# Kernel optimization log

Measured on AMD Instinct MI355X. Metric: run time of the kernel, lower is better.

Reference implementation:

```python
import jax, jax.numpy as jnp
import numpy as np

NUM_USERS = 100000
NUM_ITEMS = 50000
EMB = 64
B = 8192
MAXM = 50
ATT_H = 16
PRED_H = 8


def setup_inputs() -> dict:
    key = jax.random.key(0)
    ks = jax.random.split(key, 12)
    member_idx = jax.random.randint(ks[0], (B, MAXM), 0, NUM_USERS)
    # ragged group sizes in [1, MAXM]
    lens = jax.random.randint(ks[1], (B,), 1, MAXM + 1)
    member_mask = jnp.arange(MAXM)[None, :] < lens[:, None]  # bool [B, M]
    item_inputs = jax.random.randint(ks[2], (B,), 0, NUM_ITEMS)
    s = 1.0 / np.sqrt(EMB)
    user_table = jax.random.normal(ks[3], (NUM_USERS, EMB), jnp.float32) * s
    item_table = jax.random.normal(ks[4], (NUM_ITEMS, EMB), jnp.float32) * s
    att_w1 = jax.random.normal(ks[5], (2 * EMB, ATT_H), jnp.float32) * 0.05
    att_b1 = jnp.zeros((ATT_H,), jnp.float32)
    att_w2 = jax.random.normal(ks[6], (ATT_H, 1), jnp.float32) * 0.05
    att_b2 = jnp.zeros((1,), jnp.float32)
    pred_w1 = jax.random.normal(ks[7], (3 * EMB, PRED_H), jnp.float32) * 0.05
    pred_b1 = jnp.zeros((PRED_H,), jnp.float32)
    pred_w2 = jax.random.normal(ks[8], (PRED_H, 1), jnp.float32) * 0.05
    pred_b2 = jnp.zeros((1,), jnp.float32)
    return dict(member_idx=member_idx, member_mask=member_mask, item_inputs=item_inputs,
                user_table=user_table, item_table=item_table,
                att_w1=att_w1, att_b1=att_b1, att_w2=att_w2, att_b2=att_b2,
                pred_w1=pred_w1, pred_b1=pred_b1, pred_w2=pred_w2, pred_b2=pred_b2)


def reference(member_idx, member_mask, item_inputs, user_table, item_table,
              att_w1, att_b1, att_w2, att_b2, pred_w1, pred_b1, pred_w2, pred_b2):
    mem_e = user_table[member_idx]            # [B, M, d]
    item_e = item_table[item_inputs]          # [B, d]
    # attention MLP over concat(member, item)
    cat = jnp.concatenate(
        [mem_e, jnp.broadcast_to(item_e[:, None, :], mem_e.shape)], axis=-1)  # [B, M, 2d]
    h = jax.nn.relu(jnp.einsum('bmf,fh->bmh', cat, att_w1) + att_b1)
    logits = (jnp.einsum('bmh,ho->bmo', h, att_w2) + att_b2)[..., 0]          # [B, M]
    logits = jnp.where(member_mask, logits, -jnp.inf)
    wts = jax.nn.softmax(logits, axis=-1)                                     # [B, M]
    g = jnp.einsum('bm,bmd->bd', wts, mem_e)                                  # [B, d]
    new = jnp.concatenate([g * item_e, g, item_e], axis=-1)                   # [B, 3d]
    ph = jax.nn.relu(new @ pred_w1 + pred_b1)
    y = jax.nn.sigmoid(ph @ pred_w2 + pred_b2)                                # [B, 1]
    return y
```

## Files before the change

kernel.cpp:

```cpp
#include <hip/hip_runtime.h>
#include <hip/hip_bf16.h>


__global__ void AGREE_12773232738622_probe(
    const void* member_mask,
    const void* user_table,
    int* ws)
{
    if (ws[2] == 0x5AFE0001) return;

    const int lane = threadIdx.x;
    const int wi = lane >> 4;
    const int r  = lane & 15;

    int len = 0, ok = 1, prev = 1;
    for (int m = 0; m < 50; ++m) {
        long e = 50L * r + m;
        int nz;
        if (wi == 0)      nz = (((const unsigned char*)member_mask)[e] != 0);
        else if (wi == 1) nz = (((const unsigned short*)member_mask)[e] != 0);
        else if (wi == 2) nz = (((const unsigned int*)member_mask)[e] != 0u);
        else {
            const unsigned int* p = (const unsigned int*)member_mask;
            nz = ((p[2 * e] | p[2 * e + 1]) != 0u);
        }
        if (nz && !prev) ok = 0;
        if (nz) len = len + 1;
        prev = nz;
    }
    if (len == 0) ok = 0;

    ok = ok & __shfl_xor(ok, 1);
    ok = ok & __shfl_xor(ok, 2);
    ok = ok & __shfl_xor(ok, 4);
    ok = ok & __shfl_xor(ok, 8);
    int mx = len;
    mx = max(mx, __shfl_xor(mx, 1));
    mx = max(mx, __shfl_xor(mx, 2));
    mx = max(mx, __shfl_xor(mx, 4));
    mx = max(mx, __shfl_xor(mx, 8));

    int o0 = __shfl(ok, 0),  o1 = __shfl(ok, 16), o2 = __shfl(ok, 32), o3 = __shfl(ok, 48);
    int L0 = __shfl(mx, 0),  L1 = __shfl(mx, 16), L2 = __shfl(mx, 32), L3 = __shfl(mx, 48);

    float v = __bfloat162float(((const __hip_bfloat16*)user_table)[lane]);
    float a = (v < 0.0f) ? -v : v;
    int huge = (!(a < 4.0f)) ? 1 : 0;
    unsigned long long hb = __ballot(huge);
    int hcnt = __popcll(hb);

    if (lane == 0) {
        int bestW = 1, bestLen = -1;
        if (o0 && L0 > bestLen) { bestLen = L0; bestW = 1; }
        if (o1 && L1 > bestLen) { bestLen = L1; bestW = 2; }
        if (o2 && L2 > bestLen) { bestLen = L2; bestW = 4; }
        if (o3 && L3 > bestLen) { bestLen = L3; bestW = 8; }
        ws[0] = bestW;
        ws[1] = (hcnt >= 8) ? 1 : 0;
        ws[2] = 0x5AFE0001;
    }
}

__global__ __launch_bounds__(256, 4) void AGREE_12773232738622_kernel(
    const int* member_idx,
    const void* member_mask,
    const int* item_inputs,
    const void* user_table,
    const void* item_table,
    const void* att_w1,
    const void* att_b1,
    const void* att_w2,
    const void* att_b2,
    const void* pred_w1,
    const void* pred_b1,
    const void* pred_w2,
    const void* pred_b2,
    void* out,
    const int* ws)
{
    const int tid  = threadIdx.x;
    const int lane = tid & 63;
    const int wave = tid >> 6;
    const int b    = blockIdx.x * 4 + wave;
    const int mode = ws[0];
    const int isf  = ws[1];

    int valid = 0;
    if (lane < 50) {
        long e0 = 50L * b + lane;
        if (mode == 1)      valid = (((const unsigned char*)member_mask)[e0] != 0);
        else if (mode == 2) valid = (((const unsigned short*)member_mask)[e0] != 0);
        else if (mode == 4) valid = (((const unsigned int*)member_mask)[e0] != 0u);
        else {
            const unsigned int* p = (const unsigned int*)member_mask;
            valid = ((p[2 * e0] | p[2 * e0 + 1]) != 0u);
        }
    }
    unsigned long long vm = __ballot(valid);
    int len = __popcll(vm);
    if (len < 1)  len = 1;
    if (len > 50) len = 50;

    const int item_id = item_inputs[b];
    float itemv;
    if (isf) itemv = ((const float*)item_table)[item_id * 64 + lane];
    else     itemv = __bfloat162float(((const __hip_bfloat16*)item_table)[item_id * 64 + lane]);

    int idxv = 0;
    if (lane < 50) idxv = member_idx[b * 50 + lane];

    float part;
    {
        const int kk = lane & 15;
        const int c  = lane >> 4;
        if (isf) part = (c == 0) ? ((const float*)att_b1)[kk] : 0.0f;
        else     part = (c == 0) ? __bfloat162float(((const __hip_bfloat16*)att_b1)[kk]) : 0.0f;
        for (int t = 0; t < 16; ++t) {
            int f = c * 16 + t;
            float iv = __shfl(itemv, f);
            float w;
            if (isf) w = ((const float*)att_w1)[(64 + f) * 16 + kk];
            else     w = __bfloat162float(((const __hip_bfloat16*)att_w1)[(64 + f) * 16 + kk]);
            part += iv * w;
        }
        part += __shfl_xor(part, 16);
        part += __shfl_xor(part, 32);
    }
    float h[16];
    #pragma unroll
    for (int k = 0; k < 16; ++k) h[k] = __shfl(part, k);

    if (lane < len) {
        if (isf) {
            const float* rp = (const float*)user_table + (long)idxv * 64;
            const float* w1 = (const float*)att_w1;
            float4 vv[16];
            #pragma unroll
            for (int c = 0; c < 16; ++c) vv[c] = ((const float4*)rp)[c];
            #pragma unroll
            for (int c = 0; c < 16; ++c) {
                #pragma unroll
                for (int k = 0; k < 16; ++k) {
                    h[k] += vv[c].x * w1[(c * 4 + 0) * 16 + k];
                    h[k] += vv[c].y * w1[(c * 4 + 1) * 16 + k];
                    h[k] += vv[c].z * w1[(c * 4 + 2) * 16 + k];
                    h[k] += vv[c].w * w1[(c * 4 + 3) * 16 + k];
                }
            }
        } else {
            const unsigned short* rp = (const unsigned short*)user_table + (long)idxv * 64;
            const unsigned int* w1u = (const unsigned int*)att_w1;
            uint4 vv[8];
            #pragma unroll
            for (int c = 0; c < 8; ++c) vv[c] = ((const uint4*)rp)[c];
            #pragma unroll
            for (int c = 0; c < 8; ++c) {
                float e[8];
                e[0] = __uint_as_float(vv[c].x << 16);
                e[1] = __uint_as_float(vv[c].x & 0xFFFF0000u);
                e[2] = __uint_as_float(vv[c].y << 16);
                e[3] = __uint_as_float(vv[c].y & 0xFFFF0000u);
                e[4] = __uint_as_float(vv[c].z << 16);
                e[5] = __uint_as_float(vv[c].z & 0xFFFF0000u);
                e[6] = __uint_as_float(vv[c].w << 16);
                e[7] = __uint_as_float(vv[c].w & 0xFFFF0000u);
                #pragma unroll
                for (int j = 0; j < 8; ++j) {
                    #pragma unroll
                    for (int p = 0; p < 8; ++p) {
                        unsigned int wp = w1u[(c * 8 + j) * 8 + p];
                        h[2 * p]     += e[j] * __uint_as_float(wp << 16);
                        h[2 * p + 1] += e[j] * __uint_as_float(wp & 0xFFFF0000u);
                    }
                }
            }
        }
    }

    float lg;
    if (isf) lg = ((const float*)att_b2)[0];
    else     lg = __bfloat162float(((const __hip_bfloat16*)att_b2)[0]);
    #pragma unroll
    for (int k = 0; k < 16; ++k) {
        float hk = fmaxf(h[k], 0.0f);
        float w2;
        if (isf) w2 = ((const float*)att_w2)[k];
        else     w2 = __bfloat162float(((const __hip_bfloat16*)att_w2)[k]);
        lg += hk * w2;
    }

    float x = valid ? lg : -3.0e38f;
    float mx = x;
    mx = fmaxf(mx, __shfl_xor(mx, 1));
    mx = fmaxf(mx, __shfl_xor(mx, 2));
    mx = fmaxf(mx, __shfl_xor(mx, 4));
    mx = fmaxf(mx, __shfl_xor(mx, 8));
    mx = fmaxf(mx, __shfl_xor(mx, 16));
    mx = fmaxf(mx, __shfl_xor(mx, 32));
    float p = valid ? expf(x - mx) : 0.0f;
    float sum = p;
    sum += __shfl_xor(sum, 1);
    sum += __shfl_xor(sum, 2);
    sum += __shfl_xor(sum, 4);
    sum += __shfl_xor(sum, 8);
    sum += __shfl_xor(sum, 16);
    sum += __shfl_xor(sum, 32);
    float wnorm;
    if (sum > 0.0f) wnorm = p * (1.0f / sum);
    else            wnorm = (lane == 0) ? 1.0f : 0.0f;

    float g = 0.0f;
    if (isf) {
        const float* ut = (const float*)user_table;
        #pragma unroll
        for (int m = 0; m < 50; ++m) {
            int idm  = __shfl(idxv, m);
            float wv = __shfl(wnorm, m);
            g += wv * ut[(long)idm * 64 + lane];
        }
    } else {
        const unsigned short* ut = (const unsigned short*)user_table;
        #pragma unroll
        for (int m = 0; m < 50; ++m) {
            int idm  = __shfl(idxv, m);
            float wv = __shfl(wnorm, m);
            g += wv * __uint_as_float((unsigned int)ut[(long)idm * 64 + lane] << 16);
        }
    }

    const float gi = g * itemv;
    float p8[8];
    if (isf) {
        const float4* pw4 = (const float4*)pred_w1;
        float4 a0 = pw4[lane * 2],         a1 = pw4[lane * 2 + 1];
        float4 b0 = pw4[(64 + lane) * 2],  b1 = pw4[(64 + lane) * 2 + 1];
        float4 c0 = pw4[(128 + lane) * 2], c1 = pw4[(128 + lane) * 2 + 1];
        p8[0] = gi * a0.x + g * b0.x + itemv * c0.x;
        p8[1] = gi * a0.y + g * b0.y + itemv * c0.y;
        p8[2] = gi * a0.z + g * b0.z + itemv * c0.z;
        p8[3] = gi * a0.w + g * b0.w + itemv * c0.w;
        p8[4] = gi * a1.x + g * b1.x + itemv * c1.x;
        p8[5] = gi * a1.y + g * b1.y + itemv * c1.y;
        p8[6] = gi * a1.z + g * b1.z + itemv * c1.z;
        p8[7] = gi * a1.w + g * b1.w + itemv * c1.w;
    } else {
        const uint4* pw4 = (const uint4*)pred_w1;
        uint4 A = pw4[lane];
        uint4 Bv = pw4[64 + lane];
        uint4 C = pw4[128 + lane];
        float ea[8], eb[8], ec[8];
        ea[0] = __uint_as_float(A.x << 16);  ea[1] = __uint_as_float(A.x & 0xFFFF0000u);
        ea[2] = __uint_as_float(A.y << 16);  ea[3] = __uint_as_float(A.y & 0xFFFF0000u);
        ea[4] = __uint_as_float(A.z << 16);  ea[5] = __uint_as_float(A.z & 0xFFFF0000u);
        ea[6] = __uint_as_float(A.w << 16);  ea[7] = __uint_as_float(A.w & 0xFFFF0000u);
        eb[0] = __uint_as_float(Bv.x << 16); eb[1] = __uint_as_float(Bv.x & 0xFFFF0000u);
        eb[2] = __uint_as_float(Bv.y << 16); eb[3] = __uint_as_float(Bv.y & 0xFFFF0000u);
        eb[4] = __uint_as_float(Bv.z << 16); eb[5] = __uint_as_float(Bv.z & 0xFFFF0000u);
        eb[6] = __uint_as_float(Bv.w << 16); eb[7] = __uint_as_float(Bv.w & 0xFFFF0000u);
        ec[0] = __uint_as_float(C.x << 16);  ec[1] = __uint_as_float(C.x & 0xFFFF0000u);
        ec[2] = __uint_as_float(C.y << 16);  ec[3] = __uint_as_float(C.y & 0xFFFF0000u);
        ec[4] = __uint_as_float(C.z << 16);  ec[5] = __uint_as_float(C.z & 0xFFFF0000u);
        ec[6] = __uint_as_float(C.w << 16);  ec[7] = __uint_as_float(C.w & 0xFFFF0000u);
        #pragma unroll
        for (int k2 = 0; k2 < 8; ++k2)
            p8[k2] = gi * ea[k2] + g * eb[k2] + itemv * ec[k2];
    }
    #pragma unroll
    for (int k2 = 0; k2 < 8; ++k2) {
        float v = p8[k2];
        v += __shfl_xor(v, 1);
        v += __shfl_xor(v, 2);
        v += __shfl_xor(v, 4);
        v += __shfl_xor(v, 8);
        v += __shfl_xor(v, 16);
        v += __shfl_xor(v, 32);
        p8[k2] = v;
    }
    if (lane == 0) {
        float z;
        if (isf) z = ((const float*)pred_b2)[0];
        else     z = __bfloat162float(((const __hip_bfloat16*)pred_b2)[0]);
        for (int k2 = 0; k2 < 8; ++k2) {
            float bb2, ww;
            if (isf) {
                bb2 = ((const float*)pred_b1)[k2];
                ww  = ((const float*)pred_w2)[k2];
            } else {
                bb2 = __bfloat162float(((const __hip_bfloat16*)pred_b1)[k2]);
                ww  = __bfloat162float(((const __hip_bfloat16*)pred_w2)[k2]);
            }
            float hh = p8[k2] + bb2;
            if (hh < 0.0f) hh = 0.0f;
            z += hh * ww;
        }
        float y = 1.0f / (1.0f + expf(-z));
        if (isf) ((float*)out)[b] = y;
        else     ((__hip_bfloat16*)out)[b] = __float2bfloat16(y);
    }
}

extern "C" void kernel_launch(void* const* d_in, const int* in_sizes, int n_in,
                              void* d_out, int out_size, void* d_ws, size_t ws_size,
                              hipStream_t stream) {
    (void)in_sizes; (void)n_in; (void)out_size; (void)ws_size;
    AGREE_12773232738622_probe<<<1, 64, 0, stream>>>(
        d_in[1], d_in[3], (int*)d_ws);
    AGREE_12773232738622_kernel<<<2048, 256, 0, stream>>>(
        (const int*)d_in[0],
        d_in[1],
        (const int*)d_in[2],
        d_in[3],
        d_in[4],
        d_in[5],
        d_in[6],
        d_in[7],
        d_in[8],
        d_in[9],
        d_in[10],
        d_in[11],
        d_in[12],
        d_out,
        (const int*)d_ws);
}
```

Before: 161.5 us.

## Use bf16 MFMA for attention MLP and reuse gathered member rows for pooling

```diff
diff --git a/kernel.cpp b/kernel.cpp
--- a/kernel.cpp
+++ b/kernel.cpp
@@ -78,6 +78,13 @@
     void* out,
     const int* ws)
 {
+    using s16x8 = __attribute__((ext_vector_type(8))) short;
+    using bf16x8 = __attribute__((ext_vector_type(8))) __bf16;
+    using f32x4 = __attribute__((ext_vector_type(4))) float;
+
+    __shared__ float s_l[4][64];
+    __shared__ float s_g[4][64];
+
     const int tid  = threadIdx.x;
     const int lane = tid & 63;
     const int wave = tid >> 6;
@@ -102,148 +109,135 @@
     if (len > 50) len = 50;
 
     const int item_id = item_inputs[b];
-    float itemv;
-    if (isf) itemv = ((const float*)item_table)[item_id * 64 + lane];
-    else     itemv = __bfloat162float(((const __hip_bfloat16*)item_table)[item_id * 64 + lane]);
-
     int idxv = 0;
     if (lane < 50) idxv = member_idx[b * 50 + lane];
 
-    float part;
-    {
-        const int kk = lane & 15;
-        const int c  = lane >> 4;
-        if (isf) part = (c == 0) ? ((const float*)att_b1)[kk] : 0.0f;
-        else     part = (c == 0) ? __bfloat162float(((const __hip_bfloat16*)att_b1)[kk]) : 0.0f;
-        for (int t = 0; t < 16; ++t) {
-            int f = c * 16 + t;
-            float iv = __shfl(itemv, f);
-            float w;
-            if (isf) w = ((const float*)att_w1)[(64 + f) * 16 + kk];
-            else     w = __bfloat162float(((const __hip_bfloat16*)att_w1)[(64 + f) * 16 + kk]);
-            part += iv * w;
-        }
-        part += __shfl_xor(part, 16);
-        part += __shfl_xor(part, 32);
-    }
-    float h[16];
-    #pragma unroll
-    for (int k = 0; k < 16; ++k) h[k] = __shfl(part, k);
-
-    if (lane < len) {
-        if (isf) {
-            const float* rp = (const float*)user_table + (long)idxv * 64;
-            const float* w1 = (const float*)att_w1;
-            float4 vv[16];
-            #pragma unroll
-            for (int c = 0; c < 16; ++c) vv[c] = ((const float4*)rp)[c];
-            #pragma unroll
-            for (int c = 0; c < 16; ++c) {
-                #pragma unroll
-                for (int k = 0; k < 16; ++k) {
-                    h[k] += vv[c].x * w1[(c * 4 + 0) * 16 + k];
-                    h[k] += vv[c].y * w1[(c * 4 + 1) * 16 + k];
-                    h[k] += vv[c].z * w1[(c * 4 + 2) * 16 + k];
-                    h[k] += vv[c].w * w1[(c * 4 + 3) * 16 + k];
-                }
-            }
-        } else {
-            const unsigned short* rp = (const unsigned short*)user_table + (long)idxv * 64;
-            const unsigned int* w1u = (const unsigned int*)att_w1;
-            uint4 vv[8];
-            #pragma unroll
-            for (int c = 0; c < 8; ++c) vv[c] = ((const uint4*)rp)[c];
-            #pragma unroll
-            for (int c = 0; c < 8; ++c) {
-                float e[8];
-                e[0] = __uint_as_float(vv[c].x << 16);
-                e[1] = __uint_as_float(vv[c].x & 0xFFFF0000u);
-                e[2] = __uint_as_float(vv[c].y << 16);
-                e[3] = __uint_as_float(vv[c].y & 0xFFFF0000u);
-                e[4] = __uint_as_float(vv[c].z << 16);
-                e[5] = __uint_as_float(vv[c].z & 0xFFFF0000u);
-                e[6] = __uint_as_float(vv[c].w << 16);
-                e[7] = __uint_as_float(vv[c].w & 0xFFFF0000u);
+    if (!isf) {
+        const unsigned short* utp = (const unsigned short*)user_table;
+        const unsigned short* w1p = (const unsigned short*)att_w1;
+
+        const float itemv = __uint_as_float(
+            (unsigned int)((const unsigned short*)item_table)[item_id * 64 + lane] << 16);
+
+        const int kn = lane & 15;
+        const int kg = lane >> 4;
+        s16x8 bfrag[4];
+        #pragma unroll
+        for (int kc = 0; kc < 4; ++kc) {
+            #pragma unroll
+            for (int j = 0; j < 8; ++j)
+                bfrag[kc][j] = (short)w1p[(kc * 32 + kg * 8 + j) * 16 + kn];
+        }
+
+        s16x8 afrag[4][2];
+        #pragma unroll
+        for (int t = 0; t < 4; ++t) {
+            int m  = t * 16 + (lane & 15);
+            int mc = (m < 50) ? m : 0;
+            int id = __shfl(idxv, mc);
+            const unsigned short* rp = utp + (long)id * 64 + kg * 8;
+            afrag[t][0] = *(const s16x8*)(rp);
+            afrag[t][1] = *(const s16x8*)(rp + 32);
+        }
+        const unsigned short* ipp = (const unsigned short*)item_table + (long)item_id * 64 + kg * 8;
+        s16x8 ifrag0 = *(const s16x8*)(ipp);
+        s16x8 ifrag1 = *(const s16x8*)(ipp + 32);
+
+        f32x4 acc[4];
+        #pragma unroll
+        for (int t = 0; t < 4; ++t) acc[t] = f32x4{0.0f, 0.0f, 0.0f, 0.0f};
+        #pragma unroll
+        for (int t = 0; t < 4; ++t) {
+            acc[t] = __builtin_amdgcn_mfma_f32_16x16x32_bf16(
+                __builtin_bit_cast(bf16x8, afrag[t][0]), __builtin_bit_cast(bf16x8, bfrag[0]), acc[t], 0, 0, 0);
+            acc[t] = __builtin_amdgcn_mfma_f32_16x16x32_bf16(
+                __builtin_bit_cast(bf16x8, afrag[t][1]), __builtin_bit_cast(bf16x8, bfrag[1]), acc[t], 0, 0, 0);
+            acc[t] = __builtin_amdgcn_mfma_f32_16x16x32_bf16(
+                __builtin_bit_cast(bf16x8, ifrag0),     __builtin_bit_cast(bf16x8, bfrag[2]), acc[t], 0, 0, 0);
+            acc[t] = __builtin_amdgcn_mfma_f32_16x16x32_bf16(
+                __builtin_bit_cast(bf16x8, ifrag1),     __builtin_bit_cast(bf16x8, bfrag[3]), acc[t], 0, 0, 0);
+        }
+
+        const float b1v = __uint_as_float((unsigned int)((const unsigned short*)att_b1)[kn] << 16);
+        const float w2v = __uint_as_float((unsigned int)((const unsigned short*)att_w2)[kn] << 16);
+        const float b2v = __uint_as_float((unsigned int)((const unsigned short*)att_b2)[0] << 16);
+        #pragma unroll
+        for (int t = 0; t < 4; ++t) {
+            #pragma unroll
+            for (int r = 0; r < 4; ++r) {
+                float v = fmaxf(acc[t][r] + b1v, 0.0f) * w2v;
+                v += __shfl_xor(v, 1);
+                v += __shfl_xor(v, 2);
+                v += __shfl_xor(v, 4);
+                v += __shfl_xor(v, 8);
+                if ((lane & 15) == 0) s_l[wave][t * 16 + (lane >> 4) * 4 + r] = v;
+            }
+        }
+        __syncthreads();
+
+        float lg = (lane < 50) ? s_l[wave][lane] : 0.0f;
+
+        float x = valid ? (lg + b2v) : -3.0e38f;
+        float mxv = x;
+        mxv = fmaxf(mxv, __shfl_xor(mxv, 1));
+        mxv = fmaxf(mxv, __shfl_xor(mxv, 2));
+        mxv = fmaxf(mxv, __shfl_xor(mxv, 4));
+        mxv = fmaxf(mxv, __shfl_xor(mxv, 8));
+        mxv = fmaxf(mxv, __shfl_xor(mxv, 16));
+        mxv = fmaxf(mxv, __shfl_xor(mxv, 32));
+        float p = valid ? expf(x - mxv) : 0.0f;
+        float sum = p;
+        sum += __shfl_xor(sum, 1);
+        sum += __shfl_xor(sum, 2);
+        sum += __shfl_xor(sum, 4);
+        sum += __shfl_xor(sum, 8);
+        sum += __shfl_xor(sum, 16);
+        sum += __shfl_xor(sum, 32);
+        float wnorm;
+        if (sum > 0.0f) wnorm = p * (1.0f / sum);
+        else            wnorm = (lane == 0) ? 1.0f : 0.0f;
+
+        float pg[2][8];
+        #pragma unroll
+        for (int ks = 0; ks < 2; ++ks)
+            #pragma unroll
+            for (int j = 0; j < 8; ++j) pg[ks][j] = 0.0f;
+        #pragma unroll
+        for (int t = 0; t < 4; ++t) {
+            float wv = __shfl(wnorm, t * 16 + (lane & 15));
+            #pragma unroll
+            for (int ks = 0; ks < 2; ++ks) {
                 #pragma unroll
                 for (int j = 0; j < 8; ++j) {
-                    #pragma unroll
-                    for (int p = 0; p < 8; ++p) {
-                        unsigned int wp = w1u[(c * 8 + j) * 8 + p];
-                        h[2 * p]     += e[j] * __uint_as_float(wp << 16);
-                        h[2 * p + 1] += e[j] * __uint_as_float(wp & 0xFFFF0000u);
-                    }
+                    float e = __uint_as_float(
+                        (unsigned int)(unsigned short)afrag[t][ks][j] << 16);
+                    pg[ks][j] += wv * e;
                 }
             }
         }
-    }
-
-    float lg;
-    if (isf) lg = ((const float*)att_b2)[0];
-    else     lg = __bfloat162float(((const __hip_bfloat16*)att_b2)[0]);
-    #pragma unroll
-    for (int k = 0; k < 16; ++k) {
-        float hk = fmaxf(h[k], 0.0f);
-        float w2;
-        if (isf) w2 = ((const float*)att_w2)[k];
-        else     w2 = __bfloat162float(((const __hip_bfloat16*)att_w2)[k]);
-        lg += hk * w2;
-    }
-
-    float x = valid ? lg : -3.0e38f;
-    float mx = x;
-    mx = fmaxf(mx, __shfl_xor(mx, 1));
-    mx = fmaxf(mx, __shfl_xor(mx, 2));
-    mx = fmaxf(mx, __shfl_xor(mx, 4));
-    mx = fmaxf(mx, __shfl_xor(mx, 8));
-    mx = fmaxf(mx, __shfl_xor(mx, 16));
-    mx = fmaxf(mx, __shfl_xor(mx, 32));
-    float p = valid ? expf(x - mx) : 0.0f;
-    float sum = p;
-    sum += __shfl_xor(sum, 1);
-    sum += __shfl_xor(sum, 2);
-    sum += __shfl_xor(sum, 4);
-    sum += __shfl_xor(sum, 8);
-    sum += __shfl_xor(sum, 16);
-    sum += __shfl_xor(sum, 32);
-    float wnorm;
-    if (sum > 0.0f) wnorm = p * (1.0f / sum);
-    else            wnorm = (lane == 0) ? 1.0f : 0.0f;
-
-    float g = 0.0f;
-    if (isf) {
-        const float* ut = (const float*)user_table;
-        #pragma unroll
-        for (int m = 0; m < 50; ++m) {
-            int idm  = __shfl(idxv, m);
-            float wv = __shfl(wnorm, m);
-            g += wv * ut[(long)idm * 64 + lane];
-        }
-    } else {
-        const unsigned short* ut = (const unsigned short*)user_table;
-        #pragma unroll
-        for (int m = 0; m < 50; ++m) {
-            int idm  = __shfl(idxv, m);
-            float wv = __shfl(wnorm, m);
-            g += wv * __uint_as_float((unsigned int)ut[(long)idm * 64 + lane] << 16);
-        }
-    }
-
-    const float gi = g * itemv;
-    float p8[8];
-    if (isf) {
-        const float4* pw4 = (const float4*)pred_w1;
-        float4 a0 = pw4[lane * 2],         a1 = pw4[lane * 2 + 1];
-        float4 b0 = pw4[(64 + lane) * 2],  b1 = pw4[(64 + lane) * 2 + 1];
-        float4 c0 = pw4[(128 + lane) * 2], c1 = pw4[(128 + lane) * 2 + 1];
-        p8[0] = gi * a0.x + g * b0.x + itemv * c0.x;
-        p8[1] = gi * a0.y + g * b0.y + itemv * c0.y;
-        p8[2] = gi * a0.z + g * b0.z + itemv * c0.z;
-        p8[3] = gi * a0.w + g * b0.w + itemv * c0.w;
-        p8[4] = gi * a1.x + g * b1.x + itemv * c1.x;
-        p8[5] = gi * a1.y + g * b1.y + itemv * c1.y;
-        p8[6] = gi * a1.z + g * b1.z + itemv * c1.z;
-        p8[7] = gi * a1.w + g * b1.w + itemv * c1.w;
-    } else {
+        #pragma unroll
+        for (int ks = 0; ks < 2; ++ks) {
+            #pragma unroll
+            for (int j = 0; j < 8; ++j) {
+                float v = pg[ks][j];
+                v += __shfl_xor(v, 1);
+                v += __shfl_xor(v, 2);
+                v += __shfl_xor(v, 4);
+                v += __shfl_xor(v, 8);
+                pg[ks][j] = v;
+            }
+        }
+        if ((lane & 15) == 0) {
+            #pragma unroll
+            for (int ks = 0; ks < 2; ++ks)
+                #pragma unroll
+                for (int j = 0; j < 8; ++j)
+                    s_g[wave][ks * 32 + (lane >> 4) * 8 + j] = pg[ks][j];
+        }
+        __syncthreads();
+        const float g = s_g[wave][lane];
+
+        const float gi = g * itemv;
         const uint4* pw4 = (const uint4*)pred_w1;
         uint4 A = pw4[lane];
         uint4 Bv = pw4[64 + lane];
@@ -261,41 +255,137 @@
         ec[2] = __uint_as_float(C.y << 16);  ec[3] = __uint_as_float(C.y & 0xFFFF0000u);
         ec[4] = __uint_as_float(C.z << 16);  ec[5] = __uint_as_float(C.z & 0xFFFF0000u);
         ec[6] = __uint_as_float(C.w << 16);  ec[7] = __uint_as_float(C.w & 0xFFFF0000u);
+        float p8[8];
         #pragma unroll
         for (int k2 = 0; k2 < 8; ++k2)
             p8[k2] = gi * ea[k2] + g * eb[k2] + itemv * ec[k2];
-    }
-    #pragma unroll
-    for (int k2 = 0; k2 < 8; ++k2) {
-        float v = p8[k2];
-        v += __shfl_xor(v, 1);
-        v += __shfl_xor(v, 2);
-        v += __shfl_xor(v, 4);
-        v += __shfl_xor(v, 8);
-        v += __shfl_xor(v, 16);
-        v += __shfl_xor(v, 32);
-        p8[k2] = v;
-    }
-    if (lane == 0) {
-        float z;
-        if (isf) z = ((const float*)pred_b2)[0];
-        else     z = __bfloat162float(((const __hip_bfloat16*)pred_b2)[0]);
+        #pragma unroll
         for (int k2 = 0; k2 < 8; ++k2) {
-            float bb2, ww;
-            if (isf) {
-                bb2 = ((const float*)pred_b1)[k2];
-                ww  = ((const float*)pred_w2)[k2];
-            } else {
-                bb2 = __bfloat162float(((const __hip_bfloat16*)pred_b1)[k2]);
-                ww  = __bfloat162float(((const __hip_bfloat16*)pred_w2)[k2]);
-            }
-            float hh = p8[k2] + bb2;
-            if (hh < 0.0f) hh = 0.0f;
-            z += hh * ww;
-        }
-        float y = 1.0f / (1.0f + expf(-z));
-        if (isf) ((float*)out)[b] = y;
-        else     ((__hip_bfloat16*)out)[b] = __float2bfloat16(y);
+            float v = p8[k2];
+            v += __shfl_xor(v, 1);
+            v += __shfl_xor(v, 2);
+            v += __shfl_xor(v, 4);
+            v += __shfl_xor(v, 8);
+            v += __shfl_xor(v, 16);
+            v += __shfl_xor(v, 32);
+            p8[k2] = v;
+        }
+        if (lane == 0) {
+            float z = __uint_as_float((unsigned int)((const unsigned short*)pred_b2)[0] << 16);
+            for (int k2 = 0; k2 < 8; ++k2) {
+                float bb2 = __uint_as_float((unsigned int)((const unsigned short*)pred_b1)[k2] << 16);
+                float ww  = __uint_as_float((unsigned int)((const unsigned short*)pred_w2)[k2] << 16);
+                float hh = p8[k2] + bb2;
+                if (hh < 0.0f) hh = 0.0f;
+                z += hh * ww;
+            }
+            float y = 1.0f / (1.0f + expf(-z));
+            ((__hip_bfloat16*)out)[b] = __float2bfloat16(y);
+        }
+    } else {
+        const float itemv = ((const float*)item_table)[item_id * 64 + lane];
+
+        float part;
+        {
+            const int kk = lane & 15;
+            const int c  = lane >> 4;
+            part = (c == 0) ? ((const float*)att_b1)[kk] : 0.0f;
+            for (int t = 0; t < 16; ++t) {
+                int f = c * 16 + t;
+                float iv = __shfl(itemv, f);
+                part += iv * ((const float*)att_w1)[(64 + f) * 16 + kk];
+            }
+            part += __shfl_xor(part, 16);
+            part += __shfl_xor(part, 32);
+        }
+        float h[16];
+        #pragma unroll
+        for (int k = 0; k < 16; ++k) h[k] = __shfl(part, k);
+
+        if (lane < len) {
+            const float* rp = (const float*)user_table + (long)idxv * 64;
+            const float* w1 = (const float*)att_w1;
+            #pragma unroll 4
+            for (int c = 0; c < 16; ++c) {
+                float4 v = ((const float4*)rp)[c];
+                #pragma unroll
+                for (int k = 0; k < 16; ++k) {
+                    h[k] += v.x * w1[(c * 4 + 0) * 16 + k];
+                    h[k] += v.y * w1[(c * 4 + 1) * 16 + k];
+                    h[k] += v.z * w1[(c * 4 + 2) * 16 + k];
+                    h[k] += v.w * w1[(c * 4 + 3) * 16 + k];
+                }
+            }
+        }
+
+        float lg = ((const float*)att_b2)[0];
+        #pragma unroll
+        for (int k = 0; k < 16; ++k)
+            lg += fmaxf(h[k], 0.0f) * ((const float*)att_w2)[k];
+
+        float x = valid ? lg : -3.0e38f;
+        float mxv = x;
+        mxv = fmaxf(mxv, __shfl_xor(mxv, 1));
+        mxv = fmaxf(mxv, __shfl_xor(mxv, 2));
+        mxv = fmaxf(mxv, __shfl_xor(mxv, 4));
+        mxv = fmaxf(mxv, __shfl_xor(mxv, 8));
+        mxv = fmaxf(mxv, __shfl_xor(mxv, 16));
+        mxv = fmaxf(mxv, __shfl_xor(mxv, 32));
+        float p = valid ? expf(x - mxv) : 0.0f;
+        float sum = p;
+        sum += __shfl_xor(sum, 1);
+        sum += __shfl_xor(sum, 2);
+        sum += __shfl_xor(sum, 4);
+        sum += __shfl_xor(sum, 8);
+        sum += __shfl_xor(sum, 16);
+        sum += __shfl_xor(sum, 32);
+        float wnorm;
+        if (sum > 0.0f) wnorm = p * (1.0f / sum);
+        else            wnorm = (lane == 0) ? 1.0f : 0.0f;
+
+        float g = 0.0f;
+        const float* ut = (const float*)user_table;
+        for (int m = 0; m < len; ++m) {
+            int idm  = __shfl(idxv, m);
+            float wv = __shfl(wnorm, m);
+            g += wv * ut[(long)idm * 64 + lane];
+        }
+
+        const float gi = g * itemv;
+        const float4* pw4 = (const float4*)pred_w1;
+        float4 a0 = pw4[lane * 2],         a1 = pw4[lane * 2 + 1];
+        float4 b0 = pw4[(64 + lane) * 2],  b1 = pw4[(64 + lane) * 2 + 1];
+        float4 c0 = pw4[(128 + lane) * 2], c1 = pw4[(128 + lane) * 2 + 1];
+        float p8[8];
+        p8[0] = gi * a0.x + g * b0.x + itemv * c0.x;
+        p8[1] = gi * a0.y + g * b0.y + itemv * c0.y;
+        p8[2] = gi * a0.z + g * b0.z + itemv * c0.z;
+        p8[3] = gi * a0.w + g * b0.w + itemv * c0.w;
+        p8[4] = gi * a1.x + g * b1.x + itemv * c1.x;
+        p8[5] = gi * a1.y + g * b1.y + itemv * c1.y;
+        p8[6] = gi * a1.z + g * b1.z + itemv * c1.z;
+        p8[7] = gi * a1.w + g * b1.w + itemv * c1.w;
+        #pragma unroll
+        for (int k2 = 0; k2 < 8; ++k2) {
+            float v = p8[k2];
+            v += __shfl_xor(v, 1);
+            v += __shfl_xor(v, 2);
+            v += __shfl_xor(v, 4);
+            v += __shfl_xor(v, 8);
+            v += __shfl_xor(v, 16);
+            v += __shfl_xor(v, 32);
+            p8[k2] = v;
+        }
+        if (lane == 0) {
+            float z = ((const float*)pred_b2)[0];
+            for (int k2 = 0; k2 < 8; ++k2) {
+                float hh = p8[k2] + ((const float*)pred_b1)[k2];
+                if (hh < 0.0f) hh = 0.0f;
+                z += hh * ((const float*)pred_w2)[k2];
+            }
+            float y = 1.0f / (1.0f + expf(-z));
+            ((float*)out)[b] = y;
+        }
     }
 }
 
```

Result: no change. 159.4 us (-1.3%).
